# Performance work log

Measured on AMD Instinct MI355X. Metric: run time of the kernel, lower is better.

## Reference

```python
import jax, jax.numpy as jnp
import numpy as np

H = 16      # num heads
DH = 64     # head dim
D = H * DH  # hidden = 1024

def setup_inputs() -> dict:
    key = jax.random.key(0)
    ks = jax.random.split(key, 8)
    B, S = 4, 2048
    scale = 1.0 / np.sqrt(D)
    return {
        "hidden_states": jax.random.normal(ks[0], (B, S, D), dtype=jnp.float32),
        "attention_mask": jnp.zeros((B, S, S), dtype=jnp.float32),
        "Wq": jax.random.normal(ks[1], (D, D), dtype=jnp.float32) * scale,
        "bq": jnp.zeros((D,), dtype=jnp.float32),
        "Wk": jax.random.normal(ks[2], (D, D), dtype=jnp.float32) * scale,
        "bk": jnp.zeros((D,), dtype=jnp.float32),
        "Wv": jax.random.normal(ks[3], (D, D), dtype=jnp.float32) * scale,
        "bv": jnp.zeros((D,), dtype=jnp.float32),
    }

def _split_heads(x):
    B, S, _ = x.shape
    return x.reshape(B, S, H, DH).transpose(0, 2, 1, 3)  # [B,H,S,dh]

def reference(hidden_states, attention_mask, Wq, bq, Wk, bk, Wv, bv):
    q = _split_heads(hidden_states @ Wq + bq)
    k = _split_heads(hidden_states @ Wk + bk)
    v = _split_heads(hidden_states @ Wv + bv)
    scores = jnp.einsum("bhqd,bhkd->bhqk", q, k) / jnp.sqrt(jnp.float32(DH))
    scores = scores + attention_mask[:, None, :, :]
    probs = jax.nn.softmax(scores, axis=-1)  # dropout p=0 (eval) -> identity
    ctx = jnp.einsum("bhqk,bhkd->bhqd", probs, v)
    B, _, S, _ = ctx.shape
    return ctx.transpose(0, 2, 1, 3).reshape(B, S, H * DH)
```

## Files before the change

kernel.cpp:

```cpp
#include <hip/hip_runtime.h>

typedef __bf16 bf16;
typedef __bf16 bf16x8 __attribute__((ext_vector_type(8)));
typedef __bf16 bf16x4 __attribute__((ext_vector_type(4)));
typedef float floatx4 __attribute__((ext_vector_type(4)));

typedef __attribute__((address_space(1))) void gvoid;
typedef __attribute__((address_space(3))) void lvoid;
#define ASYNC_COPY16(gp, lp) \
  __builtin_amdgcn_global_load_lds((gvoid*)(gp), (lvoid*)(lp), 16, 0, 0)

#define NB 4
#define SQ 2048
#define DMODEL 1024
#define NH 16
#define HD 64
#define MTOK (NB * SQ)
#define LOG2E 1.44269504088896f

#define XB_OFF 0ull
#define WT_OFF (16ull * 1024 * 1024)
#define Q_OFF  (22ull * 1024 * 1024)
#define K_OFF  (38ull * 1024 * 1024)
#define V_OFF  (54ull * 1024 * 1024)
#define FLG_OFF (70ull * 1024 * 1024)

__global__ __launch_bounds__(256) void prep(
    const float* __restrict__ x, bf16* __restrict__ xb,
    const float* __restrict__ w0, const float* __restrict__ w1,
    const float* __restrict__ w2, bf16* __restrict__ wt) {
  __shared__ float tlds[32][33];
  int blk = blockIdx.x;
  int t = threadIdx.x;
  if (blk < 8192) {
    int i = blk * 256 + t;
    float4 v = ((const float4*)x)[i];
    bf16x4 o;
    o[0] = (bf16)v.x; o[1] = (bf16)v.y; o[2] = (bf16)v.z; o[3] = (bf16)v.w;
    ((bf16x4*)xb)[i] = o;
  } else {
    int tidx = blk - 8192;
    int z = tidx >> 10;
    int rem = tidx & 1023;
    int kb = ((rem >> 5) & 31) * 32, nb = (rem & 31) * 32;
    const float* w = (z == 0) ? w0 : (z == 1) ? w1 : w2;
    bf16* out = wt + (size_t)z * DMODEL * DMODEL;
    int tx = t & 31, ty = t >> 5;
#pragma unroll
    for (int i = 0; i < 4; i++)
      tlds[ty + 8 * i][tx] = w[(size_t)(kb + ty + 8 * i) * DMODEL + nb + tx];
    __syncthreads();
#pragma unroll
    for (int i = 0; i < 4; i++)
      out[(size_t)(nb + ty + 8 * i) * DMODEL + kb + tx] = (bf16)tlds[tx][ty + 8 * i];
  }
}

#define BK 64
__global__ __launch_bounds__(256) void qkv_mask(
    const bf16* __restrict__ xb,
    const bf16* __restrict__ wt,
    const float* __restrict__ biasq, const float* __restrict__ biask,
    const float* __restrict__ biasv,
    bf16* __restrict__ q, bf16* __restrict__ k, bf16* __restrict__ v,
    const float* __restrict__ mask, int* __restrict__ flags) {
  __shared__ bf16 As[128 * BK];
  __shared__ bf16 Bs[128 * BK];

  int idx = blockIdx.x;
  int r7 = idx % 7, d7 = idx / 7;
  int t = threadIdx.x;

  if (r7 >= 3) {
    int midx = d7 * 4 + (r7 - 3);
    int kt = midx & 31, qt = (midx >> 5) & 15, b = midx >> 9;
    const float* mb = mask + ((size_t)b * SQ + qt * 128) * SQ + kt * 64;
    int row = t >> 1, half = t & 1;
    const float4* p = (const float4*)(mb + (size_t)row * SQ + half * 32);
    bool nz = false;
#pragma unroll
    for (int i = 0; i < 8; i++) {
      float4 vv = p[i];
      nz |= (vv.x != 0.f) | (vv.y != 0.f) | (vv.z != 0.f) | (vv.w != 0.f);
    }
    int* acc = (int*)As;
    if (t == 0) acc[0] = 0;
    __syncthreads();
    unsigned long long m = __ballot(nz);
    if ((t & 63) == 0 && m) atomicOr(acc, 1);
    __syncthreads();
    if (t == 0) flags[(b * 16 + qt) * 32 + kt] = acc[0];
    return;
  }

  int qidx = d7 * 3 + r7;
  int mt = qidx & 63;
  int nt = qidx >> 6;
  int mat = nt >> 3;
  int nbase = (nt & 7) * 128;
  const bf16* wmat = wt + (size_t)mat * DMODEL * DMODEL;
  const float* bias = (mat == 0) ? biasq : (mat == 1) ? biask : biasv;
  bf16* outp = (mat == 0) ? q : (mat == 1) ? k : v;

  int lane = t & 63, wid = t >> 6;
  int quad = lane >> 4, l16 = lane & 15;
  int wm = (wid & 1) * 64, wn = (wid >> 1) * 64;
  int xq = quad ^ (l16 & 7);

  floatx4 acc[4][4] = {};

  for (int kb = 0; kb < DMODEL; kb += BK) {
    __syncthreads();
#pragma unroll
    for (int p = 0; p < 4; p++) {
      int i2 = p * 256 + t;
      int row = i2 >> 3;
      int gch = (i2 ^ row) & 7;
      ASYNC_COPY16(xb + (size_t)(mt * 128 + row) * DMODEL + kb + gch * 8,
                   As + i2 * 8);
      ASYNC_COPY16(wmat + (size_t)(nbase + row) * DMODEL + kb + gch * 8,
                   Bs + i2 * 8);
    }
    __syncthreads();

#pragma unroll
    for (int kc = 0; kc < BK; kc += 32) {
      int xc = (kc >> 3) ^ xq;
      bf16x8 af[4], bfr[4];
#pragma unroll
      for (int mi = 0; mi < 4; mi++)
        af[mi] = *(const bf16x8*)(As + (wm + mi * 16 + l16) * BK + xc * 8);
#pragma unroll
      for (int ni = 0; ni < 4; ni++)
        bfr[ni] = *(const bf16x8*)(Bs + (wn + ni * 16 + l16) * BK + xc * 8);
      if (mat < 2) {
#pragma unroll
        for (int mi = 0; mi < 4; mi++)
#pragma unroll
          for (int ni = 0; ni < 4; ni++)
            acc[mi][ni] = __builtin_amdgcn_mfma_f32_16x16x32_bf16(
                bfr[ni], af[mi], acc[mi][ni], 0, 0, 0);
      } else {
#pragma unroll
        for (int mi = 0; mi < 4; mi++)
#pragma unroll
          for (int ni = 0; ni < 4; ni++)
            acc[mi][ni] = __builtin_amdgcn_mfma_f32_16x16x32_bf16(
                af[mi], bfr[ni], acc[mi][ni], 0, 0, 0);
      }
    }
  }

  int mg0 = mt * 128 + wm;
  if (mat < 2) {
    float qscale = (mat == 0) ? 0.125f * LOG2E : 1.0f;
#pragma unroll
    for (int ni = 0; ni < 4; ni++) {
      int n0 = nbase + wn + ni * 16 + quad * 4;
      int h = n0 >> 6, d0 = n0 & 63;
      float4 bv4 = *(const float4*)(bias + n0);
#pragma unroll
      for (int mi = 0; mi < 4; mi++) {
        int m = mg0 + mi * 16 + l16;
        int b = m >> 11, s = m & 2047;
        bf16x4 pk;
        pk[0] = (bf16)((acc[mi][ni][0] + bv4.x) * qscale);
        pk[1] = (bf16)((acc[mi][ni][1] + bv4.y) * qscale);
        pk[2] = (bf16)((acc[mi][ni][2] + bv4.z) * qscale);
        pk[3] = (bf16)((acc[mi][ni][3] + bv4.w) * qscale);
        *(bf16x4*)(outp + (((size_t)(b * NH + h) * SQ + s) << 6) + d0) = pk;
      }
    }
  } else {
#pragma unroll
    for (int ni = 0; ni < 4; ni++) {
      int n = nbase + wn + ni * 16 + l16;
      int h = n >> 6, d = n & 63;
      float bv_ = bias[n];
#pragma unroll
      for (int mi = 0; mi < 4; mi++) {
        int m0 = mg0 + mi * 16 + quad * 4;
        int b = m0 >> 11, s = m0 & 2047;
        bf16x4 pk;
#pragma unroll
        for (int r = 0; r < 4; r++) pk[r] = (bf16)(acc[mi][ni][r] + bv_);
        *(bf16x4*)(outp + (((size_t)(b * NH + h) * HD + d) << 11) + s) = pk;
      }
    }
  }
}

#define PPAD 72
__global__ __launch_bounds__(256, 4) void attn(
    const bf16* __restrict__ Q,
    const bf16* __restrict__ K,
    const bf16* __restrict__ Vt,
    const float* __restrict__ mask,
    const int* __restrict__ flags,
    float* __restrict__ out) {
  __shared__ bf16 Ks[64 * 64];
  __shared__ bf16 Vs[64 * 64];
  __shared__ bf16 P[4][32][PPAD];

  int bh = blockIdx.x;
  int qt = blockIdx.y;
  int b = bh >> 4, h = bh & 15;
  int t = threadIdx.x, lane = t & 63, wid = t >> 6;
  int quad = lane >> 4, l16 = lane & 15;
  int q0 = qt * 128 + wid * 32;

  const bf16* Qp = Q + ((size_t)bh * SQ + q0) * HD;
  const bf16* Kp = K + (size_t)bh * SQ * HD;
  const bf16* Vp = Vt + (size_t)bh * HD * SQ;
  const float* mp = mask + ((size_t)b * SQ + q0) * SQ;
  const int* flg = flags + (b * 16 + qt) * 32;

  bf16x8 qa[2][2];
#pragma unroll
  for (int m = 0; m < 2; m++) {
    const bf16* qr = Qp + (size_t)(m * 16 + l16) * HD;
    qa[m][0] = *(const bf16x8*)(qr + quad * 8);
    qa[m][1] = *(const bf16x8*)(qr + 32 + quad * 8);
  }

  floatx4 o[2][4] = {};
  float li[2] = {0.f, 0.f};
  bf16* Pw = &P[wid][0][0];
  int xq = quad ^ (l16 & 7);

  for (int kb = 0, kti = 0; kb < SQ; kb += 64, kti++) {
    __syncthreads();
#pragma unroll
    for (int p = 0; p < 2; p++) {
      int idx = p * 256 + t;
      int row = idx >> 3;
      int gch = (idx ^ row) & 7;
      ASYNC_COPY16(Kp + (size_t)(kb + row) * HD + gch * 8, Ks + idx * 8);
      ASYNC_COPY16(Vp + (size_t)row * SQ + kb + gch * 8, Vs + idx * 8);
    }
    __syncthreads();
    int flag = flg[kti];

    float xs[2][4][4];
#pragma unroll
    for (int kt = 0; kt < 4; kt++) {
      const bf16* kr = Ks + (kt * 16 + l16) * 64;
      bf16x8 k0 = *(const bf16x8*)(kr + xq * 8);
      bf16x8 k1 = *(const bf16x8*)(kr + (xq ^ 4) * 8);
      floatx4 z0 = {}, z1 = {};
      z0 = __builtin_amdgcn_mfma_f32_16x16x32_bf16(k0, qa[0][0], z0, 0, 0, 0);
      z0 = __builtin_amdgcn_mfma_f32_16x16x32_bf16(k1, qa[0][1], z0, 0, 0, 0);
      z1 = __builtin_amdgcn_mfma_f32_16x16x32_bf16(k0, qa[1][0], z1, 0, 0, 0);
      z1 = __builtin_amdgcn_mfma_f32_16x16x32_bf16(k1, qa[1][1], z1, 0, 0, 0);
#pragma unroll
      for (int r = 0; r < 4; r++) { xs[0][kt][r] = z0[r]; xs[1][kt][r] = z1[r]; }
    }
    if (flag) {
#pragma unroll
      for (int m = 0; m < 2; m++)
#pragma unroll
        for (int kt = 0; kt < 4; kt++)
#pragma unroll
          for (int r = 0; r < 4; r++)
            xs[m][kt][r] = __builtin_fmaf(
                mp[(size_t)(m * 16 + l16) * SQ + kb + kt * 16 + quad * 4 + r],
                LOG2E, xs[m][kt][r]);
    }

#pragma unroll
    for (int m = 0; m < 2; m++) {
      float sum = 0.f;
#pragma unroll
      for (int kt = 0; kt < 4; kt++) {
        bf16x4 pk;
#pragma unroll
        for (int r = 0; r < 4; r++) {
          float e = __builtin_amdgcn_exp2f(xs[m][kt][r]);
          sum += e;
          pk[r] = (bf16)e;
        }
        *(bf16x4*)(Pw + (m * 16 + l16) * PPAD + kt * 16 + quad * 4) = pk;
      }
      li[m] += sum;
    }
    asm volatile("s_waitcnt lgkmcnt(0)" ::: "memory");
    bf16x8 pb[2][2];
#pragma unroll
    for (int m = 0; m < 2; m++) {
      pb[m][0] = *(const bf16x8*)(Pw + (m * 16 + l16) * PPAD + quad * 8);
      pb[m][1] = *(const bf16x8*)(Pw + (m * 16 + l16) * PPAD + 32 + quad * 8);
    }

#pragma unroll
    for (int dt = 0; dt < 4; dt++) {
      const bf16* vr = Vs + (dt * 16 + l16) * 64;
      bf16x8 v0 = *(const bf16x8*)(vr + xq * 8);
      bf16x8 v1 = *(const bf16x8*)(vr + (xq ^ 4) * 8);
      o[0][dt] = __builtin_amdgcn_mfma_f32_16x16x32_bf16(v0, pb[0][0], o[0][dt], 0, 0, 0);
      o[0][dt] = __builtin_amdgcn_mfma_f32_16x16x32_bf16(v1, pb[0][1], o[0][dt], 0, 0, 0);
      o[1][dt] = __builtin_amdgcn_mfma_f32_16x16x32_bf16(v0, pb[1][0], o[1][dt], 0, 0, 0);
      o[1][dt] = __builtin_amdgcn_mfma_f32_16x16x32_bf16(v1, pb[1][1], o[1][dt], 0, 0, 0);
    }
  }
#pragma unroll
  for (int m = 0; m < 2; m++) {
    li[m] += __shfl_xor(li[m], 16, 64);
    li[m] += __shfl_xor(li[m], 32, 64);
  }
#pragma unroll
  for (int m = 0; m < 2; m++) {
    float inv = 1.0f / li[m];
    float* op = out + ((size_t)b * SQ + q0 + m * 16 + l16) * DMODEL + h * HD;
#pragma unroll
    for (int dt = 0; dt < 4; dt++)
#pragma unroll
      for (int r = 0; r < 4; r++)
        op[dt * 16 + quad * 4 + r] = o[m][dt][r] * inv;
  }
}

extern "C" void kernel_launch(void* const* d_in, const int* in_sizes, int n_in,
                              void* d_out, int out_size, void* d_ws, size_t ws_size,
                              hipStream_t stream) {
  (void)in_sizes; (void)n_in; (void)out_size; (void)ws_size;
  const float* hs   = (const float*)d_in[0];
  const float* mask = (const float*)d_in[1];
  const float* Wq   = (const float*)d_in[2];
  const float* bq   = (const float*)d_in[3];
  const float* Wk   = (const float*)d_in[4];
  const float* bk   = (const float*)d_in[5];
  const float* Wv   = (const float*)d_in[6];
  const float* bv   = (const float*)d_in[7];
  float* out = (float*)d_out;
  char* ws = (char*)d_ws;
  bf16* xb = (bf16*)(ws + XB_OFF);
  bf16* wt = (bf16*)(ws + WT_OFF);
  bf16* q  = (bf16*)(ws + Q_OFF);
  bf16* k  = (bf16*)(ws + K_OFF);
  bf16* v  = (bf16*)(ws + V_OFF);
  int* flg = (int*)(ws + FLG_OFF);

  prep<<<8192 + 3072, 256, 0, stream>>>(hs, xb, Wq, Wk, Wv, wt);
  qkv_mask<<<3584, 256, 0, stream>>>(xb, wt, bq, bk, bv, q, k, v, mask, flg);
  attn<<<dim3(64, 16), 256, 0, stream>>>(q, k, v, mask, flg, out);
}
```

Baseline: 298.2 us.

## Move mask scan into prep, swizzle QKV GEMM tiles, raise MFMA wave priority

The mask-nonzero scan blocks move out of the QKV GEMM kernel and into the prep kernel, so the GEMM launch holds only matmul tiles. Those tiles are remapped so that neighbouring blocks share weight columns across different row tiles, which should improve L2 reuse. In the attention loop, s_setprio raises wave priority around the two MFMA sections so matrix work is issued ahead of the softmax arithmetic from other waves. The cost is a longer prep kernel that now also reads the full mask.

```diff
diff --git a/kernel.cpp b/kernel.cpp
--- a/kernel.cpp
+++ b/kernel.cpp
@@ -28,7 +28,8 @@
 __global__ __launch_bounds__(256) void prep(
     const float* __restrict__ x, bf16* __restrict__ xb,
     const float* __restrict__ w0, const float* __restrict__ w1,
-    const float* __restrict__ w2, bf16* __restrict__ wt) {
+    const float* __restrict__ w2, bf16* __restrict__ wt,
+    const float* __restrict__ mask, int* __restrict__ flags) {
   __shared__ float tlds[32][33];
   int blk = blockIdx.x;
   int t = threadIdx.x;
@@ -38,7 +39,7 @@
     bf16x4 o;
     o[0] = (bf16)v.x; o[1] = (bf16)v.y; o[2] = (bf16)v.z; o[3] = (bf16)v.w;
     ((bf16x4*)xb)[i] = o;
-  } else {
+  } else if (blk < 11264) {
     int tidx = blk - 8192;
     int z = tidx >> 10;
     int rem = tidx & 1023;
@@ -53,26 +54,8 @@
 #pragma unroll
     for (int i = 0; i < 4; i++)
       out[(size_t)(nb + ty + 8 * i) * DMODEL + kb + tx] = (bf16)tlds[tx][ty + 8 * i];
-  }
-}
-
-#define BK 64
-__global__ __launch_bounds__(256) void qkv_mask(
-    const bf16* __restrict__ xb,
-    const bf16* __restrict__ wt,
-    const float* __restrict__ biasq, const float* __restrict__ biask,
-    const float* __restrict__ biasv,
-    bf16* __restrict__ q, bf16* __restrict__ k, bf16* __restrict__ v,
-    const float* __restrict__ mask, int* __restrict__ flags) {
-  __shared__ bf16 As[128 * BK];
-  __shared__ bf16 Bs[128 * BK];
-
-  int idx = blockIdx.x;
-  int r7 = idx % 7, d7 = idx / 7;
-  int t = threadIdx.x;
-
-  if (r7 >= 3) {
-    int midx = d7 * 4 + (r7 - 3);
+  } else {
+    int midx = blk - 11264;
     int kt = midx & 31, qt = (midx >> 5) & 15, b = midx >> 9;
     const float* mb = mask + ((size_t)b * SQ + qt * 128) * SQ + kt * 64;
     int row = t >> 1, half = t & 1;
@@ -83,19 +66,32 @@
       float4 vv = p[i];
       nz |= (vv.x != 0.f) | (vv.y != 0.f) | (vv.z != 0.f) | (vv.w != 0.f);
     }
-    int* acc = (int*)As;
+    int* acc = (int*)tlds;
     if (t == 0) acc[0] = 0;
     __syncthreads();
     unsigned long long m = __ballot(nz);
     if ((t & 63) == 0 && m) atomicOr(acc, 1);
     __syncthreads();
     if (t == 0) flags[(b * 16 + qt) * 32 + kt] = acc[0];
-    return;
-  }
-
-  int qidx = d7 * 3 + r7;
-  int mt = qidx & 63;
-  int nt = qidx >> 6;
+  }
+}
+
+#define BK 64
+__global__ __launch_bounds__(256) void qkv(
+    const bf16* __restrict__ xb,
+    const bf16* __restrict__ wt,
+    const float* __restrict__ biasq, const float* __restrict__ biask,
+    const float* __restrict__ biasv,
+    bf16* __restrict__ q, bf16* __restrict__ k, bf16* __restrict__ v) {
+  __shared__ bf16 As[128 * BK];
+  __shared__ bf16 Bs[128 * BK];
+
+  int id = blockIdx.x;
+  int local = id >> 3;
+  int mt = ((id & 7) << 3) | (local & 7);
+  int nt = local >> 3;
+  int t = threadIdx.x;
+
   int mat = nt >> 3;
   int nbase = (nt & 7) * 128;
   const bf16* wmat = wt + (size_t)mat * DMODEL * DMODEL;
@@ -242,6 +238,7 @@
     int flag = flg[kti];
 
     float xs[2][4][4];
+    __builtin_amdgcn_s_setprio(1);
 #pragma unroll
     for (int kt = 0; kt < 4; kt++) {
       const bf16* kr = Ks + (kt * 16 + l16) * 64;
@@ -255,6 +252,7 @@
 #pragma unroll
       for (int r = 0; r < 4; r++) { xs[0][kt][r] = z0[r]; xs[1][kt][r] = z1[r]; }
     }
+    __builtin_amdgcn_s_setprio(0);
     if (flag) {
 #pragma unroll
       for (int m = 0; m < 2; m++)
@@ -291,6 +289,7 @@
       pb[m][1] = *(const bf16x8*)(Pw + (m * 16 + l16) * PPAD + 32 + quad * 8);
     }
 
+    __builtin_amdgcn_s_setprio(1);
 #pragma unroll
     for (int dt = 0; dt < 4; dt++) {
       const bf16* vr = Vs + (dt * 16 + l16) * 64;
@@ -301,6 +300,7 @@
       o[1][dt] = __builtin_amdgcn_mfma_f32_16x16x32_bf16(v0, pb[1][0], o[1][dt], 0, 0, 0);
       o[1][dt] = __builtin_amdgcn_mfma_f32_16x16x32_bf16(v1, pb[1][1], o[1][dt], 0, 0, 0);
     }
+    __builtin_amdgcn_s_setprio(0);
   }
 #pragma unroll
   for (int m = 0; m < 2; m++) {
@@ -340,7 +340,7 @@
   bf16* v  = (bf16*)(ws + V_OFF);
   int* flg = (int*)(ws + FLG_OFF);
 
-  prep<<<8192 + 3072, 256, 0, stream>>>(hs, xb, Wq, Wk, Wv, wt);
-  qkv_mask<<<3584, 256, 0, stream>>>(xb, wt, bq, bk, bv, q, k, v, mask, flg);
+  prep<<<8192 + 3072 + 2048, 256, 0, stream>>>(hs, xb, Wq, Wk, Wv, wt, mask, flg);
+  qkv<<<1536, 256, 0, stream>>>(xb, wt, bq, bk, bv, q, k, v);
   attn<<<dim3(64, 16), 256, 0, stream>>>(q, k, v, mask, flg, out);
 }
```

Result: no change. 301.8 us (+1.2%).
